# Kernel tuning notes

Hardware: AMD Instinct MI355X
Metric: run time of the kernel (lower is better)

## Reference

```python
import jax, jax.numpy as jnp
import numpy as np

B, S, D_IN, D_MODEL, H = 2, 2048, 1024, 1024, 16
DEPTH = D_MODEL // H


def setup_inputs() -> dict:
    key = jax.random.key(0)
    ks = jax.random.split(key, 12)
    f32 = jnp.float32
    scale = 0.02  # typical init scale for linear weights
    inp = {
        "v": jax.random.normal(ks[0], (B, S, D_IN), f32),
        "k": jax.random.normal(ks[1], (B, S, D_IN), f32),
        "q": jax.random.normal(ks[2], (B, S, D_IN), f32),
        # padding mask: 1 -> masked out, 0 -> keep; broadcastable to (B,H,Sq,Sk)
        "mask": jax.random.randint(ks[3], (B, 1, 1, S), 0, 2).astype(f32),
        # linear params stored as [in, out] so y = x @ W + b (matches torch Linear math)
        "Wq": jax.random.normal(ks[4], (D_IN, D_MODEL), f32) * scale,
        "bq": jnp.zeros((D_MODEL,), f32),
        "Wk": jax.random.normal(ks[5], (D_IN, D_MODEL), f32) * scale,
        "bk": jnp.zeros((D_MODEL,), f32),
        "Wv": jax.random.normal(ks[6], (D_IN, D_MODEL), f32) * scale,
        "bv": jnp.zeros((D_MODEL,), f32),
        "Wo": jax.random.normal(ks[7], (D_MODEL, D_MODEL), f32) * scale,
        "bo": jnp.zeros((D_MODEL,), f32),
    }
    return inp


def _split_heads(x):
    # [B, S, D_MODEL] -> [B, H, S, DEPTH]
    b = x.shape[0]
    return x.reshape(b, -1, H, DEPTH).transpose(0, 2, 1, 3)


def reference(v, k, q, mask, Wq, bq, Wk, bk, Wv, bv, Wo, bo):
    qh = _split_heads(q @ Wq + bq)   # [B,H,Sq,D]
    kh = _split_heads(k @ Wk + bk)   # [B,H,Sk,D]
    vh = _split_heads(v @ Wv + bv)   # [B,H,Sk,D]

    # scaled dot-product attention with additive mask (mask * -1e9)
    inv_sqrt_dk = 1.0 / jnp.sqrt(jnp.float32(DEPTH))
    logits = jnp.einsum('bhqd,bhkd->bhqk', qh, kh) * inv_sqrt_dk
    logits = logits + mask * (-1e9)
    attn = jax.nn.softmax(logits, axis=-1)          # [B,H,Sq,Sk]
    ctx = jnp.einsum('bhqk,bhkd->bhqd', attn, vh)   # [B,H,Sq,D]

    b = q.shape[0]
    concat = ctx.transpose(0, 2, 1, 3).reshape(b, -1, D_MODEL)  # [B,Sq,D_MODEL]
    out = concat @ Wo + bo
    return out, attn
```

## Files before the change

### kernel.cpp

```cpp
#include <hip/hip_runtime.h>
#include <cstdint>
#include <cstddef>

typedef __attribute__((ext_vector_type(4))) float f4;
typedef __attribute__((ext_vector_type(8))) short bf16x8;
typedef __attribute__((ext_vector_type(8))) unsigned short u16x8;
typedef unsigned long long u64;

__device__ __forceinline__ unsigned short f2bf(float x) {
    unsigned u = __float_as_uint(x);
    u += 0x7fffu + ((u >> 16) & 1u);
    return (unsigned short)(u >> 16);
}
__device__ __forceinline__ float bf2f(unsigned short h) {
    return __uint_as_float(((unsigned)h) << 16);
}
__device__ __forceinline__ float fast_exp2(float x) { return __builtin_amdgcn_exp2f(x); }
__device__ __forceinline__ float fast_log2(float x) { return __builtin_amdgcn_logf(x); }
__device__ __forceinline__ void gll16(const void* g, void* l) {
    __builtin_amdgcn_global_load_lds(
        (const __attribute__((address_space(1))) unsigned int*)g,
        (__attribute__((address_space(3))) unsigned int*)l, 16, 0, 0);
}
__device__ __forceinline__ f4 mfma16(bf16x8 a, bf16x8 b, f4 c) {
    return __builtin_amdgcn_mfma_f32_16x16x32_bf16(a, b, c, 0, 0, 0);
}

__global__ __launch_bounds__(256)
void prep_w_kernel(const float* __restrict__ Wq, const float* __restrict__ Wk,
                   const float* __restrict__ Wv, const float* __restrict__ Wo,
                   unsigned short* __restrict__ wt)
{
    const int w = blockIdx.z;
    const float* W = w == 0 ? Wq : (w == 1 ? Wk : (w == 2 ? Wv : Wo));
    unsigned short* hi = wt + (size_t)w * 1048576;

    const int kb = blockIdx.x << 6, nb = blockIdx.y << 6;
    __shared__ float T[64][68];
    const int tid = threadIdx.x;
    {
        const int r = tid >> 2, c0 = (tid & 3) << 4;
        const float* src = W + (size_t)(kb + r) * 1024 + nb + c0;
        *(f4*)&T[r][c0 + 0]  = *(const f4*)(src + 0);
        *(f4*)&T[r][c0 + 4]  = *(const f4*)(src + 4);
        *(f4*)&T[r][c0 + 8]  = *(const f4*)(src + 8);
        *(f4*)&T[r][c0 + 12] = *(const f4*)(src + 12);
    }
    __syncthreads();
    {
        const int n = tid & 63, ks = (tid >> 6) << 4;
        unsigned short vh[16];
        #pragma unroll
        for (int j = 0; j < 16; ++j) vh[j] = f2bf(T[ks + j][n]);
        const size_t dst = (size_t)(nb + n) * 1024 + kb + ks;
        *(u16x8*)(hi + dst)     = *(u16x8*)&vh[0];
        *(u16x8*)(hi + dst + 8) = *(u16x8*)&vh[8];
    }
}

__global__ __launch_bounds__(256)
void prep_a_kernel(const float* __restrict__ q, const float* __restrict__ k,
                   const float* __restrict__ v, unsigned short* __restrict__ a_hi)
{
    const int gid = blockIdx.x * 256 + threadIdx.x;
    const int z = gid >> 18;
    const int rem = gid & 262143;
    const float* src = z == 0 ? q : (z == 1 ? k : v);
    const size_t off = (size_t)rem << 4;
    const float* s = src + off;
    unsigned short* hi = a_hi + ((size_t)z << 22) + off;
    float xs[16];
    *(f4*)&xs[0]  = *(const f4*)(s + 0);
    *(f4*)&xs[4]  = *(const f4*)(s + 4);
    *(f4*)&xs[8]  = *(const f4*)(s + 8);
    *(f4*)&xs[12] = *(const f4*)(s + 12);
    unsigned short hv[16];
    #pragma unroll
    for (int j = 0; j < 16; ++j) hv[j] = f2bf(xs[j]);
    *(u16x8*)(hi + 0) = *(u16x8*)&hv[0];
    *(u16x8*)(hi + 8) = *(u16x8*)&hv[8];
}

__global__ __launch_bounds__(256)
void vtr_kernel(const unsigned short* __restrict__ v_hi, unsigned short* __restrict__ vT)
{
    __shared__ unsigned short T[64][80];
    const int bh = blockIdx.y;
    const int s0 = blockIdx.x << 6;
    const int tid = threadIdx.x;
    const size_t base = (size_t)bh * 131072;
    {
        const int s = tid >> 2, dq = (tid & 3) << 4;
        const unsigned short* src = v_hi + base + (size_t)(s0 + s) * 64 + dq;
        u16x8 a = *(const u16x8*)src;
        u16x8 b = *(const u16x8*)(src + 8);
        *(u16x8*)&T[s][dq]     = a;
        *(u16x8*)&T[s][dq + 8] = b;
    }
    __syncthreads();
    {
        const int d = tid >> 2, sq = (tid & 3) << 4;
        unsigned short o[16];
        #pragma unroll
        for (int j = 0; j < 16; ++j) o[j] = T[sq + j][d];
        unsigned short* dst = vT + base + ((size_t)d << 11) + s0 + sq;
        *(u16x8*)dst       = *(u16x8*)&o[0];
        *(u16x8*)(dst + 8) = *(u16x8*)&o[8];
    }
}

__device__ __forceinline__ void gemm1_core(
    const unsigned short* __restrict__ AH, const unsigned short* __restrict__ WH,
    const float* __restrict__ bias, int bm, int bn, int mode,
    unsigned short* __restrict__ o_hi, float* __restrict__ o_f32, unsigned char* lds)
{
    unsigned char* As = lds;
    unsigned char* Bs = lds + 16384;

    const int tid = threadIdx.x, lane = tid & 63, wave = tid >> 6;
    const int wm = wave >> 1, wn = wave & 1;
    const int cx = lane & 15, lg = lane >> 4;
    const int l3 = lane >> 3, p3 = lane & 7;
    const int m0 = bm << 7, n0 = bn << 7;

    f4 acc[4][4];
    #pragma unroll
    for (int i = 0; i < 4; ++i)
        #pragma unroll
        for (int j = 0; j < 4; ++j) acc[i][j] = (f4){0.f, 0.f, 0.f, 0.f};

    #pragma unroll 1
    for (int k0 = 0; k0 < 1024; k0 += 64) {
        __syncthreads();
        #pragma unroll
        for (int c = 0; c < 4; ++c) {
            const int cb = (c << 2) + wave;
            const int row = (cb << 3) + l3;
            const int lgx = p3 ^ (row & 7);
            gll16(AH + (size_t)(m0 + row) * 1024 + k0 + (lgx << 3),
                  As + (cb << 10) + (lane << 4));
            gll16(WH + (size_t)(n0 + row) * 1024 + k0 + (lgx << 3),
                  Bs + (cb << 10) + (lane << 4));
        }
        __syncthreads();
        #pragma unroll
        for (int ks = 0; ks < 2; ++ks) {
            bf16x8 ah[4], bh[4];
            #pragma unroll
            for (int t = 0; t < 4; ++t) {
                const int r = (wm << 6) + (t << 4) + cx;
                ah[t] = *(const bf16x8*)(As + r * 128 + (((((ks << 2) + lg)) ^ (r & 7)) << 4));
                const int n = (wn << 6) + (t << 4) + cx;
                bh[t] = *(const bf16x8*)(Bs + n * 128 + (((((ks << 2) + lg)) ^ (n & 7)) << 4));
            }
            #pragma unroll
            for (int i = 0; i < 4; ++i)
                #pragma unroll
                for (int j = 0; j < 4; ++j)
                    acc[i][j] = mfma16(ah[i], bh[j], acc[i][j]);
        }
    }

    float bv4[4];
    #pragma unroll
    for (int j = 0; j < 4; ++j) bv4[j] = bias[n0 + (wn << 6) + (j << 4) + cx];

    #pragma unroll
    for (int i = 0; i < 4; ++i)
        #pragma unroll
        for (int j = 0; j < 4; ++j) {
            const int n = n0 + (wn << 6) + (j << 4) + cx;
            const int mb = m0 + (wm << 6) + (i << 4) + (lg << 2);
            if (mode == 2) {
                #pragma unroll
                for (int r = 0; r < 4; ++r)
                    o_f32[(size_t)(mb + r) * 1024 + n] = acc[i][j][r] + bv4[j];
            } else {
                const int b = mb >> 11, hh = n >> 6, d = n & 63;
                #pragma unroll
                for (int r = 0; r < 4; ++r) {
                    const int s = (mb + r) & 2047;
                    o_hi[(((size_t)(b * 16 + hh)) * 2048 + s) * 64 + d] = f2bf(acc[i][j][r] + bv4[j]);
                }
            }
        }
}

__global__ __launch_bounds__(256)
void qkv_gemm_kernel(const unsigned short* __restrict__ a_hi,
                     const unsigned short* __restrict__ wt,
                     const float* __restrict__ bq, const float* __restrict__ bk,
                     const float* __restrict__ bv,
                     unsigned short* __restrict__ q_hi, unsigned short* __restrict__ k_hi,
                     unsigned short* __restrict__ v_hi)
{
    __shared__ __align__(16) unsigned char lds[32768];
    const int f = blockIdx.x;
    const int id2 = (f & 7) * 96 + (f >> 3);
    const int z = id2 >> 8;
    const int rem = id2 & 255;
    const int bn = rem >> 5, bm = rem & 31;
    const unsigned short* AH = a_hi + ((size_t)z << 22);
    const unsigned short* WH = wt + (size_t)z * 1048576;
    const float* bias = z == 0 ? bq : (z == 1 ? bk : bv);
    unsigned short* ohi = z == 0 ? q_hi : (z == 1 ? k_hi : v_hi);
    gemm1_core(AH, WH, bias, bm, bn, 1, ohi, nullptr, lds);
}

__global__ __launch_bounds__(256)
void out_gemm_kernel(const unsigned short* __restrict__ ctx_hi,
                     const unsigned short* __restrict__ wt_o,
                     const float* __restrict__ bo, float* __restrict__ out)
{
    __shared__ __align__(16) unsigned char lds[32768];
    const int f = blockIdx.x;
    const int id2 = (f & 7) * 32 + (f >> 3);
    const int bn = id2 >> 5, bm = id2 & 31;
    gemm1_core(ctx_hi, wt_o, bo, bm, bn, 2, nullptr, out, lds);
}

__global__ __launch_bounds__(256, 4)
void attn_kernel(const unsigned short* __restrict__ q_hi, const unsigned short* __restrict__ k_hi,
                 const unsigned short* __restrict__ vT, const float* __restrict__ mask,
                 float* __restrict__ attn, unsigned short* __restrict__ ctx_hi)
{
    __shared__ __align__(16) unsigned char lds[40960];
    unsigned char* K1 = lds;
    unsigned char* Vs = lds + 16384;
    unsigned char* Ps = lds + 32768;

    const int f = blockIdx.x;
    const int swzf = (f & 7) * 128 + (f >> 3);
    const int bh = swzf >> 5;
    const int q0 = (swzf & 31) << 6;
    const int b = bh >> 4, h = bh & 15;
    const int tid = threadIdx.x, lane = tid & 63, wave = tid >> 6;
    const int cx = lane & 15, lg = lane >> 4;
    const int l3 = lane >> 3, p3 = lane & 7;
    const size_t base = (size_t)bh * 131072;
    const float* mg = mask + (size_t)b * 2048;

    constexpr float C2   = 0.18033688011112042f;
    constexpr float M2   = -1.4426950408889634e9f;
    constexpr float MFIX = 4.0f;

    #pragma unroll
    for (int c = 0; c < 2; ++c) {
        const int cb = (c << 2) + wave;
        const int row = (cb << 3) + l3;
        const int lgx = p3 ^ (row & 7);
        gll16(q_hi + base + (size_t)(q0 + row) * 64 + (lgx << 3),
              Ps + (cb << 10) + (lane << 4));
        gll16(k_hi + base + (size_t)row * 64 + (lgx << 3),
              K1 + (cb << 10) + (lane << 4));
    }
    f4 mrc[4];
    #pragma unroll
    for (int nt = 0; nt < 4; ++nt) mrc[nt] = *(const f4*)(mg + (nt << 4) + (lg << 2));
    asm volatile("s_waitcnt vmcnt(0)" ::: "memory");
    __builtin_amdgcn_s_barrier();

    bf16x8 qb[2];
    {
        const int r = (wave << 4) + cx;
        const int mk = r & 7;
        #pragma unroll
        for (int ks = 0; ks < 2; ++ks)
            qb[ks] = *(const bf16x8*)(Ps + r * 128 + (((((ks << 2) + lg)) ^ mk) << 4));
    }

    float l4[4] = {0.f, 0.f, 0.f, 0.f};
    #pragma unroll 1
    for (int t = 0; t < 32; ++t) {
        const int p = t & 1;
        const int k0 = t << 6;
        f4 mrn[4];
        if (t < 31) {
            #pragma unroll
            for (int c = 0; c < 2; ++c) {
                const int cb = (c << 2) + wave;
                const int row = (cb << 3) + l3;
                const int lgx = p3 ^ (row & 7);
                gll16(k_hi + base + (size_t)(k0 + 64 + row) * 64 + (lgx << 3),
                      K1 + ((p ^ 1) << 13) + (cb << 10) + (lane << 4));
            }
            __builtin_amdgcn_sched_barrier(0);
            #pragma unroll
            for (int nt = 0; nt < 4; ++nt)
                mrn[nt] = *(const f4*)(mg + k0 + 64 + (nt << 4) + (lg << 2));
        }
        const unsigned char* Kc = K1 + (p << 13);
        __builtin_amdgcn_s_setprio(1);
        f4 sv[4];
        #pragma unroll
        for (int nt = 0; nt < 4; ++nt) {
            const int kr = (nt << 4) + cx;
            const int mk = kr & 7;
            f4 s = (f4){0.f, 0.f, 0.f, 0.f};
            #pragma unroll
            for (int ks = 0; ks < 2; ++ks) {
                const bf16x8 kb = *(const bf16x8*)(Kc + kr * 128 + (((((ks << 2) + lg)) ^ mk) << 4));
                s = mfma16(kb, qb[ks], s);
            }
            sv[nt] = s;
        }
        __builtin_amdgcn_s_setprio(0);
        #pragma unroll
        for (int nt = 0; nt < 4; ++nt)
            #pragma unroll
            for (int r = 0; r < 4; ++r)
                l4[nt] += fast_exp2(fmaf(sv[nt][r], C2, fmaf(mrc[nt][r], M2, -MFIX)));
        #pragma unroll
        for (int nt = 0; nt < 4; ++nt) mrc[nt] = mrn[nt];
        asm volatile("s_waitcnt vmcnt(4)" ::: "memory");
        __builtin_amdgcn_s_barrier();
    }
    float ssum = (l4[0] + l4[1]) + (l4[2] + l4[3]);
    ssum += __shfl_xor(ssum, 16);
    ssum += __shfl_xor(ssum, 32);
    const float cofs = -MFIX - fast_log2(ssum);

    #pragma unroll
    for (int c = 0; c < 2; ++c) {
        const int cb = (c << 2) + wave;
        const int row = (cb << 3) + l3;
        const int lgx = p3 ^ (row & 7);
        gll16(k_hi + base + (size_t)row * 64 + (lgx << 3),
              K1 + (cb << 10) + (lane << 4));
        gll16(vT + base + ((size_t)row << 11) + (lgx << 3),
              Vs + (cb << 10) + (lane << 4));
    }
    #pragma unroll
    for (int nt = 0; nt < 4; ++nt) mrc[nt] = *(const f4*)(mg + (nt << 4) + (lg << 2));
    asm volatile("s_waitcnt vmcnt(0)" ::: "memory");
    __builtin_amdgcn_s_barrier();

    f4 cacc[4];
    #pragma unroll
    for (int nt = 0; nt < 4; ++nt) cacc[nt] = (f4){0.f, 0.f, 0.f, 0.f};

    float* ablk = attn + ((size_t)bh * 2048 + q0) * 2048;
    const unsigned psSwz = (unsigned)((cx & 7) << 4);

    #pragma unroll 1
    for (int t = 0; t < 32; ++t) {
        const int p = t & 1;
        const int k0 = t << 6;
        f4 mrn[4];
        if (t < 31) {
            #pragma unroll
            for (int c = 0; c < 2; ++c) {
                const int cb = (c << 2) + wave;
                const int row = (cb << 3) + l3;
                const int lgx = p3 ^ (row & 7);
                gll16(k_hi + base + (size_t)(k0 + 64 + row) * 64 + (lgx << 3),
                      K1 + ((p ^ 1) << 13) + (cb << 10) + (lane << 4));
                gll16(vT + base + ((size_t)row << 11) + k0 + 64 + (lgx << 3),
                      Vs + ((p ^ 1) << 13) + (cb << 10) + (lane << 4));
            }
            #pragma unroll
            for (int nt = 0; nt < 4; ++nt)
                mrn[nt] = *(const f4*)(mg + k0 + 64 + (nt << 4) + (lg << 2));
        }
        const unsigned char* Kc = K1 + (p << 13);
        f4 s[4];
        __builtin_amdgcn_s_setprio(1);
        #pragma unroll
        for (int nt = 0; nt < 4; ++nt) {
            const int kr = (nt << 4) + cx;
            const int mk = kr & 7;
            s[nt] = (f4){0.f, 0.f, 0.f, 0.f};
            #pragma unroll
            for (int ks = 0; ks < 2; ++ks) {
                const bf16x8 kb = *(const bf16x8*)(Kc + kr * 128 + (((((ks << 2) + lg)) ^ mk) << 4));
                s[nt] = mfma16(kb, qb[ks], s[nt]);
            }
        }
        __builtin_amdgcn_s_setprio(0);
        #pragma unroll
        for (int nt = 0; nt < 4; ++nt) {
            f4 pv;
            #pragma unroll
            for (int r = 0; r < 4; ++r)
                pv[r] = fast_exp2(fmaf(s[nt][r], C2, fmaf(mrc[nt][r], M2, cofs)));
            const unsigned w0 = (unsigned)f2bf(pv[0]) | ((unsigned)f2bf(pv[1]) << 16);
            const unsigned w1 = (unsigned)f2bf(pv[2]) | ((unsigned)f2bf(pv[3]) << 16);
            const u64 packed = (u64)w0 | ((u64)w1 << 32);
            *(u64*)(Ps + (((wave << 4) + cx) * 128) +
                    ((unsigned)((nt << 5) + (lg << 3)) ^ psSwz)) = packed;
        }
        #pragma unroll
        for (int nt = 0; nt < 4; ++nt) mrc[nt] = mrn[nt];
        #pragma unroll
        for (int i = 0; i < 4; ++i) {
            const int row = (wave << 4) + (i << 2) + (lane >> 4);
            const unsigned kb = (unsigned)((lane & 15) << 3);
            const u64 pk = *(const u64*)(Ps + row * 128 + (kb ^ ((unsigned)(row & 7) << 4)));
            f4 ov;
            ov[0] = bf2f((unsigned short)(pk));
            ov[1] = bf2f((unsigned short)(pk >> 16));
            ov[2] = bf2f((unsigned short)(pk >> 32));
            ov[3] = bf2f((unsigned short)(pk >> 48));
            *(f4*)(ablk + (size_t)row * 2048 + k0 + ((lane & 15) << 2)) = ov;
        }
        __builtin_amdgcn_s_setprio(1);
        #pragma unroll
        for (int ks = 0; ks < 2; ++ks) {
            const bf16x8 pa = *(const bf16x8*)(Ps + (((wave << 4) + cx) * 128) +
                                ((unsigned)((ks << 6) + (lg << 4)) ^ psSwz));
            #pragma unroll
            for (int nt = 0; nt < 4; ++nt) {
                const int dr = (nt << 4) + cx;
                const bf16x8 vb = *(const bf16x8*)(Vs + (p << 13) + dr * 128 +
                                    (((((ks << 2) + lg)) ^ (dr & 7)) << 4));
                cacc[nt] = mfma16(pa, vb, cacc[nt]);
            }
        }
        __builtin_amdgcn_s_setprio(0);
        asm volatile("s_waitcnt vmcnt(4)" ::: "memory");
        __builtin_amdgcn_s_barrier();
    }

    #pragma unroll
    for (int nt = 0; nt < 4; ++nt)
        #pragma unroll
        for (int r = 0; r < 4; ++r) {
            const int srow = q0 + (wave << 4) + (lg << 2) + r;
            const int d = (h << 6) + (nt << 4) + cx;
            ctx_hi[((size_t)b * 2048 + srow) * 1024 + d] = f2bf(cacc[nt][r]);
        }
}

extern "C" void kernel_launch(void* const* d_in, const int* in_sizes, int n_in,
                              void* d_out, int out_size, void* d_ws, size_t ws_size,
                              hipStream_t stream)
{
    const float* v_in = (const float*)d_in[0];
    const float* k_in = (const float*)d_in[1];
    const float* q_in = (const float*)d_in[2];
    const float* mask = (const float*)d_in[3];
    const float* Wq = (const float*)d_in[4];
    const float* bq = (const float*)d_in[5];
    const float* Wk = (const float*)d_in[6];
    const float* bk = (const float*)d_in[7];
    const float* Wv = (const float*)d_in[8];
    const float* bv = (const float*)d_in[9];
    const float* Wo = (const float*)d_in[10];
    const float* bo = (const float*)d_in[11];

    float* out  = (float*)d_out;
    float* attn = out + (size_t)4194304;

    unsigned char* ws = (unsigned char*)d_ws;
    unsigned short* wt     = (unsigned short*)(ws);
    unsigned short* q_hi   = (unsigned short*)(ws + (size_t)(8)  * 1048576);
    unsigned short* k_hi   = (unsigned short*)(ws + (size_t)(16) * 1048576);
    unsigned short* v_hi   = (unsigned short*)(ws + (size_t)(24) * 1048576);
    unsigned short* ctx_hi = (unsigned short*)(ws + (size_t)(32) * 1048576);
    unsigned short* vT     = (unsigned short*)(ws + (size_t)(40) * 1048576);

    unsigned short* a_hi   = (unsigned short*)(attn + (size_t)60 * 1048576);

    prep_w_kernel<<<dim3(16, 16, 4), 256, 0, stream>>>(Wq, Wk, Wv, Wo, wt);
    prep_a_kernel<<<3072, 256, 0, stream>>>(q_in, k_in, v_in, a_hi);
    qkv_gemm_kernel<<<768, 256, 0, stream>>>(a_hi, wt, bq, bk, bv, q_hi, k_hi, v_hi);
    vtr_kernel<<<dim3(32, 32), 256, 0, stream>>>(v_hi, vT);
    attn_kernel<<<1024, 256, 0, stream>>>(q_hi, k_hi, vT, mask, attn, ctx_hi);
    out_gemm_kernel<<<256, 256, 0, stream>>>(ctx_hi, wt + (size_t)3 * 1048576, bo, out);
}
```

Baseline: 285.3 us.

## Fuse fp32-to-bf16 activation conversion into QKV GEMM and use packed bf16 convert

Drops the separate prep kernel that converted q/k/v activations to bf16. The QKV GEMM now reads fp32 activations directly and converts them while storing into swizzled LDS. This removes one launch and a full write-then-read of the bf16 copy. In exchange, the GEMM re-reads fp32 A tiles, twice the bytes, once per N block, and loads them through registers instead of async global-to-LDS. The change also replaces manual bf16 rounding with the v_cvt_pk_bf16_f32 instruction in the QKV A path and in the attention P pack, and inlines the shared GEMM core into both GEMM kernels.

```diff
diff --git a/kernel.cpp b/kernel.cpp
--- a/kernel.cpp
+++ b/kernel.cpp
@@ -14,6 +14,11 @@
 }
 __device__ __forceinline__ float bf2f(unsigned short h) {
     return __uint_as_float(((unsigned)h) << 16);
+}
+__device__ __forceinline__ unsigned cvtpk_bf16(float lo, float hi) {
+    unsigned r;
+    asm("v_cvt_pk_bf16_f32 %0, %1, %2" : "=v"(r) : "v"(lo), "v"(hi));
+    return r;
 }
 __device__ __forceinline__ float fast_exp2(float x) { return __builtin_amdgcn_exp2f(x); }
 __device__ __forceinline__ float fast_log2(float x) { return __builtin_amdgcn_logf(x); }
@@ -56,29 +61,6 @@
         *(u16x8*)(hi + dst)     = *(u16x8*)&vh[0];
         *(u16x8*)(hi + dst + 8) = *(u16x8*)&vh[8];
     }
-}
-
-__global__ __launch_bounds__(256)
-void prep_a_kernel(const float* __restrict__ q, const float* __restrict__ k,
-                   const float* __restrict__ v, unsigned short* __restrict__ a_hi)
-{
-    const int gid = blockIdx.x * 256 + threadIdx.x;
-    const int z = gid >> 18;
-    const int rem = gid & 262143;
-    const float* src = z == 0 ? q : (z == 1 ? k : v);
-    const size_t off = (size_t)rem << 4;
-    const float* s = src + off;
-    unsigned short* hi = a_hi + ((size_t)z << 22) + off;
-    float xs[16];
-    *(f4*)&xs[0]  = *(const f4*)(s + 0);
-    *(f4*)&xs[4]  = *(const f4*)(s + 4);
-    *(f4*)&xs[8]  = *(const f4*)(s + 8);
-    *(f4*)&xs[12] = *(const f4*)(s + 12);
-    unsigned short hv[16];
-    #pragma unroll
-    for (int j = 0; j < 16; ++j) hv[j] = f2bf(xs[j]);
-    *(u16x8*)(hi + 0) = *(u16x8*)&hv[0];
-    *(u16x8*)(hi + 8) = *(u16x8*)&hv[8];
 }
 
 __global__ __launch_bounds__(256)
@@ -109,85 +91,9 @@
     }
 }
 
-__device__ __forceinline__ void gemm1_core(
-    const unsigned short* __restrict__ AH, const unsigned short* __restrict__ WH,
-    const float* __restrict__ bias, int bm, int bn, int mode,
-    unsigned short* __restrict__ o_hi, float* __restrict__ o_f32, unsigned char* lds)
-{
-    unsigned char* As = lds;
-    unsigned char* Bs = lds + 16384;
-
-    const int tid = threadIdx.x, lane = tid & 63, wave = tid >> 6;
-    const int wm = wave >> 1, wn = wave & 1;
-    const int cx = lane & 15, lg = lane >> 4;
-    const int l3 = lane >> 3, p3 = lane & 7;
-    const int m0 = bm << 7, n0 = bn << 7;
-
-    f4 acc[4][4];
-    #pragma unroll
-    for (int i = 0; i < 4; ++i)
-        #pragma unroll
-        for (int j = 0; j < 4; ++j) acc[i][j] = (f4){0.f, 0.f, 0.f, 0.f};
-
-    #pragma unroll 1
-    for (int k0 = 0; k0 < 1024; k0 += 64) {
-        __syncthreads();
-        #pragma unroll
-        for (int c = 0; c < 4; ++c) {
-            const int cb = (c << 2) + wave;
-            const int row = (cb << 3) + l3;
-            const int lgx = p3 ^ (row & 7);
-            gll16(AH + (size_t)(m0 + row) * 1024 + k0 + (lgx << 3),
-                  As + (cb << 10) + (lane << 4));
-            gll16(WH + (size_t)(n0 + row) * 1024 + k0 + (lgx << 3),
-                  Bs + (cb << 10) + (lane << 4));
-        }
-        __syncthreads();
-        #pragma unroll
-        for (int ks = 0; ks < 2; ++ks) {
-            bf16x8 ah[4], bh[4];
-            #pragma unroll
-            for (int t = 0; t < 4; ++t) {
-                const int r = (wm << 6) + (t << 4) + cx;
-                ah[t] = *(const bf16x8*)(As + r * 128 + (((((ks << 2) + lg)) ^ (r & 7)) << 4));
-                const int n = (wn << 6) + (t << 4) + cx;
-                bh[t] = *(const bf16x8*)(Bs + n * 128 + (((((ks << 2) + lg)) ^ (n & 7)) << 4));
-            }
-            #pragma unroll
-            for (int i = 0; i < 4; ++i)
-                #pragma unroll
-                for (int j = 0; j < 4; ++j)
-                    acc[i][j] = mfma16(ah[i], bh[j], acc[i][j]);
-        }
-    }
-
-    float bv4[4];
-    #pragma unroll
-    for (int j = 0; j < 4; ++j) bv4[j] = bias[n0 + (wn << 6) + (j << 4) + cx];
-
-    #pragma unroll
-    for (int i = 0; i < 4; ++i)
-        #pragma unroll
-        for (int j = 0; j < 4; ++j) {
-            const int n = n0 + (wn << 6) + (j << 4) + cx;
-            const int mb = m0 + (wm << 6) + (i << 4) + (lg << 2);
-            if (mode == 2) {
-                #pragma unroll
-                for (int r = 0; r < 4; ++r)
-                    o_f32[(size_t)(mb + r) * 1024 + n] = acc[i][j][r] + bv4[j];
-            } else {
-                const int b = mb >> 11, hh = n >> 6, d = n & 63;
-                #pragma unroll
-                for (int r = 0; r < 4; ++r) {
-                    const int s = (mb + r) & 2047;
-                    o_hi[(((size_t)(b * 16 + hh)) * 2048 + s) * 64 + d] = f2bf(acc[i][j][r] + bv4[j]);
-                }
-            }
-        }
-}
-
 __global__ __launch_bounds__(256)
-void qkv_gemm_kernel(const unsigned short* __restrict__ a_hi,
+void qkv_gemm_kernel(const float* __restrict__ q_in, const float* __restrict__ k_in,
+                     const float* __restrict__ v_in,
                      const unsigned short* __restrict__ wt,
                      const float* __restrict__ bq, const float* __restrict__ bk,
                      const float* __restrict__ bv,
@@ -195,28 +101,163 @@
                      unsigned short* __restrict__ v_hi)
 {
     __shared__ __align__(16) unsigned char lds[32768];
+    unsigned char* As = lds;
+    unsigned char* Bs = lds + 16384;
+
     const int f = blockIdx.x;
     const int id2 = (f & 7) * 96 + (f >> 3);
     const int z = id2 >> 8;
     const int rem = id2 & 255;
     const int bn = rem >> 5, bm = rem & 31;
-    const unsigned short* AH = a_hi + ((size_t)z << 22);
+
+    const float* AF = z == 0 ? q_in : (z == 1 ? k_in : v_in);
     const unsigned short* WH = wt + (size_t)z * 1048576;
     const float* bias = z == 0 ? bq : (z == 1 ? bk : bv);
     unsigned short* ohi = z == 0 ? q_hi : (z == 1 ? k_hi : v_hi);
-    gemm1_core(AH, WH, bias, bm, bn, 1, ohi, nullptr, lds);
+
+    const int tid = threadIdx.x, lane = tid & 63, wave = tid >> 6;
+    const int wm = wave >> 1, wn = wave & 1;
+    const int cx = lane & 15, lg = lane >> 4;
+    const int l3 = lane >> 3, p3 = lane & 7;
+    const int m0 = bm << 7, n0 = bn << 7;
+
+    f4 acc[4][4];
+    #pragma unroll
+    for (int i = 0; i < 4; ++i)
+        #pragma unroll
+        for (int j = 0; j < 4; ++j) acc[i][j] = (f4){0.f, 0.f, 0.f, 0.f};
+
+    #pragma unroll 1
+    for (int k0 = 0; k0 < 1024; k0 += 64) {
+        __syncthreads();
+        #pragma unroll
+        for (int c = 0; c < 4; ++c) {
+            const int cb = (c << 2) + wave;
+            const int row = (cb << 3) + l3;
+            const int lgx = p3 ^ (row & 7);
+            gll16(WH + (size_t)(n0 + row) * 1024 + k0 + (lgx << 3),
+                  Bs + (cb << 10) + (lane << 4));
+        }
+        #pragma unroll
+        for (int c = 0; c < 8; ++c) {
+            const int g = (c << 8) + tid;
+            const int row = g >> 4;
+            const int k4 = g & 15;
+            const f4 av = *(const f4*)(AF + (size_t)(m0 + row) * 1024 + k0 + (k4 << 2));
+            const unsigned w0 = cvtpk_bf16(av[0], av[1]);
+            const unsigned w1 = cvtpk_bf16(av[2], av[3]);
+            const u64 pk = (u64)w0 | ((u64)w1 << 32);
+            *(u64*)(As + row * 128 + ((((k4 >> 1) ^ (row & 7)) << 4) | ((k4 & 1) << 3))) = pk;
+        }
+        __syncthreads();
+        #pragma unroll
+        for (int ks = 0; ks < 2; ++ks) {
+            bf16x8 ah[4], bh[4];
+            #pragma unroll
+            for (int t = 0; t < 4; ++t) {
+                const int r = (wm << 6) + (t << 4) + cx;
+                ah[t] = *(const bf16x8*)(As + r * 128 + (((((ks << 2) + lg)) ^ (r & 7)) << 4));
+                const int n = (wn << 6) + (t << 4) + cx;
+                bh[t] = *(const bf16x8*)(Bs + n * 128 + (((((ks << 2) + lg)) ^ (n & 7)) << 4));
+            }
+            #pragma unroll
+            for (int i = 0; i < 4; ++i)
+                #pragma unroll
+                for (int j = 0; j < 4; ++j)
+                    acc[i][j] = mfma16(ah[i], bh[j], acc[i][j]);
+        }
+    }
+
+    float bv4[4];
+    #pragma unroll
+    for (int j = 0; j < 4; ++j) bv4[j] = bias[n0 + (wn << 6) + (j << 4) + cx];
+
+    #pragma unroll
+    for (int i = 0; i < 4; ++i)
+        #pragma unroll
+        for (int j = 0; j < 4; ++j) {
+            const int n = n0 + (wn << 6) + (j << 4) + cx;
+            const int mb = m0 + (wm << 6) + (i << 4) + (lg << 2);
+            const int b = mb >> 11, hh = n >> 6, d = n & 63;
+            #pragma unroll
+            for (int r = 0; r < 4; ++r) {
+                const int s = (mb + r) & 2047;
+                ohi[(((size_t)(b * 16 + hh)) * 2048 + s) * 64 + d] = f2bf(acc[i][j][r] + bv4[j]);
+            }
+        }
 }
 
 __global__ __launch_bounds__(256)
-void out_gemm_kernel(const unsigned short* __restrict__ ctx_hi,
+void out_gemm_kernel(const unsigned short* __restrict__ AH,
                      const unsigned short* __restrict__ wt_o,
                      const float* __restrict__ bo, float* __restrict__ out)
 {
     __shared__ __align__(16) unsigned char lds[32768];
+    unsigned char* As = lds;
+    unsigned char* Bs = lds + 16384;
+
     const int f = blockIdx.x;
     const int id2 = (f & 7) * 32 + (f >> 3);
     const int bn = id2 >> 5, bm = id2 & 31;
-    gemm1_core(ctx_hi, wt_o, bo, bm, bn, 2, nullptr, out, lds);
+
+    const int tid = threadIdx.x, lane = tid & 63, wave = tid >> 6;
+    const int wm = wave >> 1, wn = wave & 1;
+    const int cx = lane & 15, lg = lane >> 4;
+    const int l3 = lane >> 3, p3 = lane & 7;
+    const int m0 = bm << 7, n0 = bn << 7;
+
+    f4 acc[4][4];
+    #pragma unroll
+    for (int i = 0; i < 4; ++i)
+        #pragma unroll
+        for (int j = 0; j < 4; ++j) acc[i][j] = (f4){0.f, 0.f, 0.f, 0.f};
+
+    #pragma unroll 1
+    for (int k0 = 0; k0 < 1024; k0 += 64) {
+        __syncthreads();
+        #pragma unroll
+        for (int c = 0; c < 4; ++c) {
+            const int cb = (c << 2) + wave;
+            const int row = (cb << 3) + l3;
+            const int lgx = p3 ^ (row & 7);
+            gll16(AH + (size_t)(m0 + row) * 1024 + k0 + (lgx << 3),
+                  As + (cb << 10) + (lane << 4));
+            gll16(wt_o + (size_t)(n0 + row) * 1024 + k0 + (lgx << 3),
+                  Bs + (cb << 10) + (lane << 4));
+        }
+        __syncthreads();
+        #pragma unroll
+        for (int ks = 0; ks < 2; ++ks) {
+            bf16x8 ah[4], bh[4];
+            #pragma unroll
+            for (int t = 0; t < 4; ++t) {
+                const int r = (wm << 6) + (t << 4) + cx;
+                ah[t] = *(const bf16x8*)(As + r * 128 + (((((ks << 2) + lg)) ^ (r & 7)) << 4));
+                const int n = (wn << 6) + (t << 4) + cx;
+                bh[t] = *(const bf16x8*)(Bs + n * 128 + (((((ks << 2) + lg)) ^ (n & 7)) << 4));
+            }
+            #pragma unroll
+            for (int i = 0; i < 4; ++i)
+                #pragma unroll
+                for (int j = 0; j < 4; ++j)
+                    acc[i][j] = mfma16(ah[i], bh[j], acc[i][j]);
+        }
+    }
+
+    float bv4[4];
+    #pragma unroll
+    for (int j = 0; j < 4; ++j) bv4[j] = bo[n0 + (wn << 6) + (j << 4) + cx];
+
+    #pragma unroll
+    for (int i = 0; i < 4; ++i)
+        #pragma unroll
+        for (int j = 0; j < 4; ++j) {
+            const int n = n0 + (wn << 6) + (j << 4) + cx;
+            const int mb = m0 + (wm << 6) + (i << 4) + (lg << 2);
+            #pragma unroll
+            for (int r = 0; r < 4; ++r)
+                out[(size_t)(mb + r) * 1024 + n] = acc[i][j][r] + bv4[j];
+        }
 }
 
 __global__ __launch_bounds__(256, 4)
@@ -383,8 +424,8 @@
             #pragma unroll
             for (int r = 0; r < 4; ++r)
                 pv[r] = fast_exp2(fmaf(s[nt][r], C2, fmaf(mrc[nt][r], M2, cofs)));
-            const unsigned w0 = (unsigned)f2bf(pv[0]) | ((unsigned)f2bf(pv[1]) << 16);
-            const unsigned w1 = (unsigned)f2bf(pv[2]) | ((unsigned)f2bf(pv[3]) << 16);
+            const unsigned w0 = cvtpk_bf16(pv[0], pv[1]);
+            const unsigned w1 = cvtpk_bf16(pv[2], pv[3]);
             const u64 packed = (u64)w0 | ((u64)w1 << 32);
             *(u64*)(Ps + (((wave << 4) + cx) * 128) +
                     ((unsigned)((nt << 5) + (lg << 3)) ^ psSwz)) = packed;
@@ -459,11 +500,9 @@
     unsigned short* ctx_hi = (unsigned short*)(ws + (size_t)(32) * 1048576);
     unsigned short* vT     = (unsigned short*)(ws + (size_t)(40) * 1048576);
 
-    unsigned short* a_hi   = (unsigned short*)(attn + (size_t)60 * 1048576);
-
     prep_w_kernel<<<dim3(16, 16, 4), 256, 0, stream>>>(Wq, Wk, Wv, Wo, wt);
-    prep_a_kernel<<<3072, 256, 0, stream>>>(q_in, k_in, v_in, a_hi);
-    qkv_gemm_kernel<<<768, 256, 0, stream>>>(a_hi, wt, bq, bk, bv, q_hi, k_hi, v_hi);
+    qkv_gemm_kernel<<<768, 256, 0, stream>>>(q_in, k_in, v_in, wt, bq, bk, bv,
+                                             q_hi, k_hi, v_hi);
     vtr_kernel<<<dim3(32, 32), 256, 0, stream>>>(v_hi, vT);
     attn_kernel<<<1024, 256, 0, stream>>>(q_hi, k_hi, vT, mask, attn, ctx_hi);
     out_gemm_kernel<<<256, 256, 0, stream>>>(ctx_hi, wt + (size_t)3 * 1048576, bo, out);
```

After: 283.1 us. No clear change (-0.8%).
